# Kernel tuning notes

Measured on AMD Instinct MI355X. Metric: run time of the kernel, lower is better.

## Reference

```python
import jax, jax.numpy as jnp
import numpy as np

NUM_VARI = 32
DIM_PER_VARI = 128  # input feature dim is 2*DIM_PER_VARI
DIM_TO = 256
BATCH = 4096
TWO_D = 2 * DIM_PER_VARI


def setup_inputs() -> dict:
    key = jax.random.key(0)
    k1, k2, k3 = jax.random.split(key, 3)
    x = jax.random.normal(k1, (NUM_VARI, BATCH, TWO_D), dtype=jnp.float32)
    # parameters, initialized like reset_parameters(): U(-std, std), std = 1/sqrt(num_vari)
    std = 1.0 / np.sqrt(NUM_VARI)
    dense_w = jax.random.uniform(k2, (NUM_VARI, 1, TWO_D, DIM_TO), dtype=jnp.float32,
                                 minval=-std, maxval=std)
    dense_bias = jax.random.uniform(k3, (NUM_VARI, 1, 1, DIM_TO), dtype=jnp.float32,
                                    minval=-std, maxval=std)
    return {"x": x, "dense_w": dense_w, "dense_bias": dense_bias}


def reference(x, dense_w, dense_bias):
    # Original: (x.unsqueeze(-1) * W + b).sum(2)
    # = grouped matmul over the feature axis + (2*dim_per_vari) * bias
    # x: [V, B, 2D], W: [V, 1, 2D, O] -> out: [V, B, O]
    out = jnp.einsum('vbd,vdo->vbo', x, dense_w[:, 0])
    out = out + TWO_D * dense_bias[:, 0]  # bias broadcast [V,1,O] -> [V,B,O]
    # activation_type == 'softplus' (original intends F.softplus)
    return jax.nn.softplus(out)
```

## Files before the change

### kernel.cpp

```cpp
#include <hip/hip_runtime.h>
#include <stdint.h>
#include <math.h>

#define NV 32
#define NB 4096
#define NK 256
#define NO 256

#define TROWS 16
#define NTILE 16

typedef __bf16 bf16x8 __attribute__((ext_vector_type(8)));
typedef float  f32x4  __attribute__((ext_vector_type(4)));

__device__ __forceinline__ f32x4 mfma16(bf16x8 a, bf16x8 b, f32x4 c) {
    return __builtin_amdgcn_mfma_f32_16x16x32_bf16(a, b, c, 0, 0, 0);
}

__device__ __forceinline__ float softplus_f(float z) {
    return fmaxf(z, 0.0f) + __logf(1.0f + __expf(-fabsf(z)));
}

__device__ __forceinline__ void gload_lds16(const void* g, void* l) {
    __builtin_amdgcn_global_load_lds((const __attribute__((address_space(1))) uint32_t*)g,
                                     (__attribute__((address_space(3))) uint32_t*)l,
                                     16, 0, 0);
}

__device__ __forceinline__ bf16x8 pin_load16(const __bf16* p) {
    bf16x8 r;
    asm volatile("global_load_dwordx4 %0, %1, off"
                 : "=v"(r) : "v"(p) : "memory");
    return r;
}

__global__ __launch_bounds__(256)
void prep_wt_kernel(const float* __restrict__ w, __bf16* __restrict__ wt) {
    const int id = blockIdx.x * 256 + threadIdx.x;
    const int o  = id & 255;
    const int kc = (id >> 8) & 31;
    const int v  = id >> 13;
    const float* src = w + ((size_t)v * NK + (size_t)kc * 8) * NO + o;
    bf16x8 r;
#pragma unroll
    for (int j = 0; j < 8; ++j) r[j] = (__bf16)src[(size_t)j * NO];
    *(bf16x8*)(wt + ((size_t)v * NO + o) * NK + kc * 8) = r;
}

__global__ __launch_bounds__(512, 4)
void mv_dense_kernel(const float* __restrict__ x, const __bf16* __restrict__ wt,
                     const float* __restrict__ bias, float* __restrict__ out) {
    __shared__ float Xs[3][TROWS * NK];

    const int t    = threadIdx.x;
    const int w    = t >> 6;
    const int lane = t & 63;
    const int lr   = lane & 15;
    const int lg   = lane >> 4;

    const int bid  = blockIdx.x;
    const int lb   = (bid & 7) * 64 + (bid >> 3);
    const int v    = lb >> 4;
    const int slab = lb & 15;

    const float* xg = x   + ((size_t)v * NB + (size_t)slab * 256) * NK;
    float*       og = out + ((size_t)v * NB + (size_t)slab * 256) * NO;

    const __bf16* wp0 = wt + ((size_t)v * NO + w * 32 + lr) * NK + lg * 8;
    const __bf16* wp1 = wp0 + (size_t)16 * NK;
    bf16x8 wv0[8], wv1[8];
#pragma unroll
    for (int kk = 0; kk < 8; ++kk) {
        wv0[kk] = pin_load16(wp0 + kk * 32);
        wv1[kk] = pin_load16(wp1 + kk * 32);
    }

    const float* bg = bias + (size_t)v * NO + w * 32 + lg * 4;
    f32x4 bb0 = *(const f32x4*)bg;
    f32x4 bb1 = *(const f32x4*)(bg + 16);
#pragma unroll
    for (int r = 0; r < 4; ++r) { bb0[r] *= 256.0f; bb1[r] *= 256.0f; }

    auto stage = [&](int tile, int buf) {
        const float* tsrc = xg + (size_t)tile * TROWS * NK;
        char* lbase = (char*)&Xs[buf][0];
#pragma unroll
        for (int d = 0; d < 2; ++d) {
            const int r = d * 8 + w;
            gload_lds16(tsrc + (size_t)r * NK + (lane ^ r) * 4,
                        (void*)(lbase + (size_t)r * 1024));
        }
    };

    auto compute = [&](int tt, const char* tb) {
        f32x4 acc0 = {0.f, 0.f, 0.f, 0.f};
        f32x4 acc1 = {0.f, 0.f, 0.f, 0.f};
#pragma unroll
        for (int kk = 0; kk < 8; ++kk) {
            const int phys = (kk * 8 + lg * 2) ^ lr;
            const char* rb = tb + (size_t)lr * 1024;
            f32x4 lo = *(const f32x4*)(rb + phys * 16);
            f32x4 hi = *(const f32x4*)(rb + (phys ^ 1) * 16);
            bf16x8 a;
#pragma unroll
            for (int e = 0; e < 4; ++e) { a[e] = (__bf16)lo[e]; a[e + 4] = (__bf16)hi[e]; }
            acc0 = mfma16(wv0[kk], a, acc0);
            acc1 = mfma16(wv1[kk], a, acc1);
        }
        float* o = og + (size_t)(tt * TROWS + lr) * NO + w * 32 + lg * 4;
        f32x4 r0, r1;
#pragma unroll
        for (int r = 0; r < 4; ++r) {
            r0[r] = softplus_f(acc0[r] + bb0[r]);
            r1[r] = softplus_f(acc1[r] + bb1[r]);
        }
        *(f32x4*)o        = r0;
        *(f32x4*)(o + 16) = r1;
    };

    stage(0, 0);
    stage(1, 1);
    asm volatile("s_waitcnt vmcnt(0)" ::: "memory");
    __builtin_amdgcn_s_barrier();
    __builtin_amdgcn_sched_barrier(0);
    stage(2, 2);
    compute(0, (const char*)&Xs[0][0]);

#pragma unroll 1
    for (int tt = 1; tt < NTILE; ++tt) {
        asm volatile("s_waitcnt vmcnt(4)" ::: "memory");
        __builtin_amdgcn_s_barrier();
        __builtin_amdgcn_sched_barrier(0);
        if (tt + 2 < NTILE) stage(tt + 2, (tt + 2) % 3);
        compute(tt, (const char*)&Xs[tt % 3][0]);
    }
}

extern "C" void kernel_launch(void* const* d_in, const int* in_sizes, int n_in,
                              void* d_out, int out_size, void* d_ws, size_t ws_size,
                              hipStream_t stream) {
    const float* x  = (const float*)d_in[0];
    const float* w  = (const float*)d_in[1];
    const float* b  = (const float*)d_in[2];
    float* out      = (float*)d_out;
    __bf16* wt      = (__bf16*)d_ws;

    hipLaunchKernelGGL(prep_wt_kernel, dim3(1024), dim3(256), 0, stream, w, wt);
    hipLaunchKernelGGL(mv_dense_kernel, dim3(512), dim3(512), 0, stream,
                       x, wt, b, out);
}
```

Measured before the change: 70.28 us.

## Halve waves per block and widen each wave to 64 output columns

Blocks drop from 8 to 4 waves. Each wave now holds weights for 64 output columns (4 MFMA chains) instead of 32, so every converted X fragment read from LDS feeds four MFMAs instead of two. This halves the LDS reads and bf16 conversions per MFMA, but doubles the weight registers per thread and changes the staging split (4 loads per wave, with the wait count adjusted to match). The higher register pressure may reduce occupancy and latency hiding.

```diff
diff --git a/kernel.cpp b/kernel.cpp
--- a/kernel.cpp
+++ b/kernel.cpp
@@ -29,8 +29,7 @@
 
 __device__ __forceinline__ bf16x8 pin_load16(const __bf16* p) {
     bf16x8 r;
-    asm volatile("global_load_dwordx4 %0, %1, off"
-                 : "=v"(r) : "v"(p) : "memory");
+    asm volatile("global_load_dwordx4 %0, %1, off" : "=v"(r) : "v"(p) : "memory");
     return r;
 }
 
@@ -47,7 +46,7 @@
     *(bf16x8*)(wt + ((size_t)v * NO + o) * NK + kc * 8) = r;
 }
 
-__global__ __launch_bounds__(512, 4)
+__global__ __launch_bounds__(256, 2)
 void mv_dense_kernel(const float* __restrict__ x, const __bf16* __restrict__ wt,
                      const float* __restrict__ bias, float* __restrict__ out) {
     __shared__ float Xs[3][TROWS * NK];
@@ -66,35 +65,38 @@
     const float* xg = x   + ((size_t)v * NB + (size_t)slab * 256) * NK;
     float*       og = out + ((size_t)v * NB + (size_t)slab * 256) * NO;
 
-    const __bf16* wp0 = wt + ((size_t)v * NO + w * 32 + lr) * NK + lg * 8;
-    const __bf16* wp1 = wp0 + (size_t)16 * NK;
-    bf16x8 wv0[8], wv1[8];
+    bf16x8 wv[4][8];
 #pragma unroll
-    for (int kk = 0; kk < 8; ++kk) {
-        wv0[kk] = pin_load16(wp0 + kk * 32);
-        wv1[kk] = pin_load16(wp1 + kk * 32);
+    for (int j = 0; j < 4; ++j) {
+        const __bf16* wp = wt + ((size_t)v * NO + w * 64 + j * 16 + lr) * NK + lg * 8;
+#pragma unroll
+        for (int kk = 0; kk < 8; ++kk)
+            wv[j][kk] = pin_load16(wp + kk * 32);
     }
 
-    const float* bg = bias + (size_t)v * NO + w * 32 + lg * 4;
-    f32x4 bb0 = *(const f32x4*)bg;
-    f32x4 bb1 = *(const f32x4*)(bg + 16);
+    f32x4 bb[4];
 #pragma unroll
-    for (int r = 0; r < 4; ++r) { bb0[r] *= 256.0f; bb1[r] *= 256.0f; }
+    for (int j = 0; j < 4; ++j)
+        bb[j] = *(const f32x4*)(bias + (size_t)v * NO + w * 64 + j * 16 + lg * 4);
 
     auto stage = [&](int tile, int buf) {
         const float* tsrc = xg + (size_t)tile * TROWS * NK;
         char* lbase = (char*)&Xs[buf][0];
 #pragma unroll
-        for (int d = 0; d < 2; ++d) {
-            const int r = d * 8 + w;
+        for (int d = 0; d < 4; ++d) {
+            const int r = d * 4 + w;
             gload_lds16(tsrc + (size_t)r * NK + (lane ^ r) * 4,
                         (void*)(lbase + (size_t)r * 1024));
         }
     };
 
     auto compute = [&](int tt, const char* tb) {
-        f32x4 acc0 = {0.f, 0.f, 0.f, 0.f};
-        f32x4 acc1 = {0.f, 0.f, 0.f, 0.f};
+        f32x4 acc[4];
+#pragma unroll
+        for (int j = 0; j < 4; ++j) {
+            f32x4 z4 = {0.f, 0.f, 0.f, 0.f};
+            acc[j] = z4;
+        }
 #pragma unroll
         for (int kk = 0; kk < 8; ++kk) {
             const int phys = (kk * 8 + lg * 2) ^ lr;
@@ -104,18 +106,19 @@
             bf16x8 a;
 #pragma unroll
             for (int e = 0; e < 4; ++e) { a[e] = (__bf16)lo[e]; a[e + 4] = (__bf16)hi[e]; }
-            acc0 = mfma16(wv0[kk], a, acc0);
-            acc1 = mfma16(wv1[kk], a, acc1);
+#pragma unroll
+            for (int j = 0; j < 4; ++j)
+                acc[j] = mfma16(wv[j][kk], a, acc[j]);
         }
-        float* o = og + (size_t)(tt * TROWS + lr) * NO + w * 32 + lg * 4;
-        f32x4 r0, r1;
+        float* op = og + (size_t)(tt * TROWS + lr) * NO + w * 64 + lg * 4;
 #pragma unroll
-        for (int r = 0; r < 4; ++r) {
-            r0[r] = softplus_f(acc0[r] + bb0[r]);
-            r1[r] = softplus_f(acc1[r] + bb1[r]);
+        for (int j = 0; j < 4; ++j) {
+            f32x4 res;
+#pragma unroll
+            for (int r = 0; r < 4; ++r)
+                res[r] = softplus_f(acc[j][r] + 256.0f * bb[j][r]);
+            *(f32x4*)(op + j * 16) = res;
         }
-        *(f32x4*)o        = r0;
-        *(f32x4*)(o + 16) = r1;
     };
 
     stage(0, 0);
@@ -128,7 +131,7 @@
 
 #pragma unroll 1
     for (int tt = 1; tt < NTILE; ++tt) {
-        asm volatile("s_waitcnt vmcnt(4)" ::: "memory");
+        asm volatile("s_waitcnt vmcnt(8)" ::: "memory");
         __builtin_amdgcn_s_barrier();
         __builtin_amdgcn_sched_barrier(0);
         if (tt + 2 < NTILE) stage(tt + 2, (tt + 2) % 3);
@@ -146,6 +149,6 @@
     __bf16* wt      = (__bf16*)d_ws;
 
     hipLaunchKernelGGL(prep_wt_kernel, dim3(1024), dim3(256), 0, stream, w, wt);
-    hipLaunchKernelGGL(mv_dense_kernel, dim3(512), dim3(512), 0, stream,
+    hipLaunchKernelGGL(mv_dense_kernel, dim3(512), dim3(256), 0, stream,
                        x, wt, b, out);
 }
```

After: 67.42 us. 1.04x faster.
